# Kernel optimization log

Hardware: AMD Instinct MI355X
Metric: run time of the kernel (lower is better)

## Reference

```python
import jax, jax.numpy as jnp
import numpy as np

B, L, D = 2, 2048, 512
H, HD = 8, 64          # num_heads, head_dim (hidden_dim = 512)
WINDOW = 256
SCALE = float(np.sqrt(HD))
LN_EPS = 1e-5


def setup_inputs() -> dict:
    key = jax.random.key(0)
    ks = jax.random.split(key, 10)
    sequence = jax.random.normal(ks[0], (B, L, D), dtype=jnp.float32)
    # lengths in [L - WINDOW//2, L] so no query row is fully masked (avoids NaN, matches original's valid regime)
    sequence_lengths = jax.random.randint(ks[1], (B,), L - WINDOW // 2, L + 1, dtype=jnp.int32)
    timestamps = jnp.sort(jax.random.uniform(ks[2], (B, L), dtype=jnp.float32) * float(L), axis=-1)
    w_std = 0.02
    Wq = jax.random.normal(ks[3], (H * HD, D), dtype=jnp.float32) * w_std
    Wk = jax.random.normal(ks[4], (H * HD, D), dtype=jnp.float32) * w_std
    Wv = jax.random.normal(ks[5], (H * HD, D), dtype=jnp.float32) * w_std
    Wo = jax.random.normal(ks[6], (D, H * HD), dtype=jnp.float32) * w_std
    bo = jnp.zeros((D,), dtype=jnp.float32)
    ln_gamma = jnp.ones((D,), dtype=jnp.float32)
    ln_beta = jnp.zeros((D,), dtype=jnp.float32)
    temporal_weight = jnp.array([0.1], dtype=jnp.float32)
    return {
        "sequence": sequence, "sequence_lengths": sequence_lengths, "timestamps": timestamps,
        "ln_gamma": ln_gamma, "ln_beta": ln_beta,
        "Wq": Wq, "Wk": Wk, "Wv": Wv, "Wo": Wo, "bo": bo,
        "temporal_weight": temporal_weight,
    }


def reference(sequence, sequence_lengths, timestamps, ln_gamma, ln_beta,
              Wq, Wk, Wv, Wo, bo, temporal_weight):
    residual = sequence
    # LayerNorm over input_dim
    mu = jnp.mean(sequence, axis=-1, keepdims=True)
    var = jnp.mean(jnp.square(sequence - mu), axis=-1, keepdims=True)
    x = (sequence - mu) * jax.lax.rsqrt(var + LN_EPS) * ln_gamma + ln_beta

    # QKV projections (spectral-normalized Linear, no bias) -> [B, L, H, HD]
    Q = (x @ Wq.T).reshape(B, L, H, HD)
    K = (x @ Wk.T).reshape(B, L, H, HD)
    V = (x @ Wv.T).reshape(B, L, H, HD)

    scores = jnp.einsum("bqhd,bkhd->bhqk", Q, K) / SCALE  # [B, H, L, L]

    # temporal decay bias
    ts_diff = jnp.abs(timestamps[:, :, None] - timestamps[:, None, :])  # [B, L, L]
    temporal_weights = jnp.exp(-jnp.abs(temporal_weight[0]) * ts_diff)
    scores = scores + jnp.log(temporal_weights + 1e-8)[:, None, :, :]

    neg_inf = jnp.float32(-jnp.inf)
    # sliding window mask (L > window_size): |i - j| <= window_size // 2
    idx = jnp.arange(L)
    wmask = jnp.abs(idx[None, :] - idx[:, None]) <= WINDOW // 2  # [L, L]
    scores = jnp.where(wmask[None, None, :, :], scores, neg_inf)

    # padding mask on key positions
    pmask = idx[None, :] < sequence_lengths[:, None]  # [B, L]
    scores = jnp.where(pmask[:, None, None, :], scores, neg_inf)

    attn = jax.nn.softmax(scores, axis=-1)  # [B, H, L, L]
    attended = jnp.einsum("bhqk,bkhd->bqhd", attn, V).reshape(B, L, H * HD)

    output = attended @ Wo.T + bo + residual  # [B, L, D]

    # exponential position-weighted aggregation over valid positions
    pos = idx.astype(jnp.float32)
    pw = jnp.exp(-0.1 * (L - 1 - pos))[None, :] * pmask.astype(jnp.float32)  # [B, L]
    pw = pw / (jnp.sum(pw, axis=1, keepdims=True) + 1e-8)
    aggregated = jnp.sum(output * pw[:, :, None], axis=1)  # [B, D]
    return aggregated
```

## Files before the change

### kernel.cpp

```cpp
#include <hip/hip_runtime.h>
#include <math.h>

#define B 2
#define L 2048
#define D 512
#define H 8
#define HD 64
#define W2 128
#define NOUT (3*D)

#define QS 1792
#define NQ (L - QS)
#define ROWS0 (QS - W2)
#define NROWS (L - ROWS0)
#define MROWS (B * NROWS)

#define TQ 4
#define NQT (NQ / TQ)

typedef __bf16 bf16_t;
typedef __attribute__((ext_vector_type(4))) __bf16 bf16x4;
typedef __attribute__((ext_vector_type(8))) __bf16 bf16x8;
typedef __attribute__((ext_vector_type(4))) float f32x4;

#define PREP_LN_BLOCKS (MROWS / 4)
#define PREP_CVT_BLOCKS 768
#define PREP_AGGS_BLOCKS 16
#define PREP_GRID (PREP_LN_BLOCKS + PREP_CVT_BLOCKS + PREP_AGGS_BLOCKS + 1)

__global__ __launch_bounds__(256) void prep_kernel(const float* __restrict__ seq,
                                                   const float* __restrict__ gamma,
                                                   const float* __restrict__ beta,
                                                   const float* __restrict__ Wq,
                                                   const float* __restrict__ Wk,
                                                   const float* __restrict__ Wv,
                                                   const int* __restrict__ slen,
                                                   bf16_t* __restrict__ xb,
                                                   bf16_t* __restrict__ wb,
                                                   float* __restrict__ aggA,
                                                   float* __restrict__ aggS) {
    int blk = blockIdx.x;
    int tid = threadIdx.x;
    int wid = tid >> 6, lane = tid & 63;

    if (blk < PREP_LN_BLOCKS) {
        int row = blk * 4 + wid;
        int b = row / NROWS;
        int l = ROWS0 + (row - b * NROWS);
        const float* src = seq + ((size_t)b * L + l) * D;
        float4 v0 = ((const float4*)src)[lane];
        float4 v1 = ((const float4*)src)[lane + 64];
        float s  = v0.x + v0.y + v0.z + v0.w + v1.x + v1.y + v1.z + v1.w;
        float sq = v0.x*v0.x + v0.y*v0.y + v0.z*v0.z + v0.w*v0.w
                 + v1.x*v1.x + v1.y*v1.y + v1.z*v1.z + v1.w*v1.w;
        for (int o = 32; o; o >>= 1) { s += __shfl_xor(s, o); sq += __shfl_xor(sq, o); }
        float mu = s * (1.0f / D);
        float var = sq * (1.0f / D) - mu * mu;
        float rstd = rsqrtf(var + 1e-5f);
        float4 g0 = ((const float4*)gamma)[lane];
        float4 g1 = ((const float4*)gamma)[lane + 64];
        float4 b0 = ((const float4*)beta)[lane];
        float4 b1 = ((const float4*)beta)[lane + 64];
        bf16x4 c0, c1;
        c0[0] = (bf16_t)((v0.x - mu) * rstd * g0.x + b0.x);
        c0[1] = (bf16_t)((v0.y - mu) * rstd * g0.y + b0.y);
        c0[2] = (bf16_t)((v0.z - mu) * rstd * g0.z + b0.z);
        c0[3] = (bf16_t)((v0.w - mu) * rstd * g0.w + b0.w);
        c1[0] = (bf16_t)((v1.x - mu) * rstd * g1.x + b1.x);
        c1[1] = (bf16_t)((v1.y - mu) * rstd * g1.y + b1.y);
        c1[2] = (bf16_t)((v1.z - mu) * rstd * g1.z + b1.z);
        c1[3] = (bf16_t)((v1.w - mu) * rstd * g1.w + b1.w);
        bf16x4* dst = (bf16x4*)(xb + (size_t)row * D);
        dst[lane] = c0;
        dst[lane + 64] = c1;
    } else if (blk < PREP_LN_BLOCKS + PREP_CVT_BLOCKS) {
        int idx = (blk - PREP_LN_BLOCKS) * 256 + tid;
        const float* src = (idx < 65536) ? Wq : (idx < 131072 ? Wk : Wv);
        int off = idx & 65535;
        float4 v = ((const float4*)src)[off];
        bf16x4 o;
        o[0] = (bf16_t)v.x; o[1] = (bf16_t)v.y; o[2] = (bf16_t)v.z; o[3] = (bf16_t)v.w;
        ((bf16x4*)wb)[idx] = o;
    } else if (blk < PREP_LN_BLOCKS + PREP_CVT_BLOCKS + PREP_AGGS_BLOCKS) {
        __shared__ float red[4][64];
        int idx = blk - (PREP_LN_BLOCKS + PREP_CVT_BLOCKS);
        int b = idx >> 3;
        int col = (idx & 7) * 64 + lane;
        int nv = slen[b] - QS;
        float s2 = 0.f;
        int i0 = wid * 64, i1 = min(i0 + 64, nv);
        for (int i = i0; i < i1; ++i) {
            float wi = __expf(-0.1f * (float)(NQ - 1 - i));
            s2 += wi * seq[((size_t)(b * L + QS + i)) * D + col];
        }
        red[wid][lane] = s2;
        __syncthreads();
        if (wid == 0) {
            aggS[b * D + col] = red[0][lane] + red[1][lane] + red[2][lane] + red[3][lane];
        }
    } else {
        ((float4*)aggA)[tid & 255] = make_float4(0.f, 0.f, 0.f, 0.f);
    }
}

__global__ __launch_bounds__(256) void qkv_gemm(const bf16_t* __restrict__ xb,
                                                const bf16_t* __restrict__ wb,
                                                float* __restrict__ qkv) {
    int m0 = blockIdx.x * 64, n0 = blockIdx.y * 64;
    int wid = threadIdx.x >> 6, lane = threadIdx.x & 63;
    int mw = m0 + (wid >> 1) * 32;
    int nw = n0 + (wid & 1) * 32;
    int mr = lane & 15, quad = lane >> 4;
    f32x4 acc00 = {}, acc01 = {}, acc10 = {}, acc11 = {};
    const bf16_t* aptr = xb + (size_t)(mw + mr) * D + quad * 8;
    const bf16_t* bptr = wb + (size_t)(nw + mr) * D + quad * 8;
#pragma unroll 4
    for (int k = 0; k < D; k += 32) {
        bf16x8 a0 = *(const bf16x8*)(aptr + k);
        bf16x8 a1 = *(const bf16x8*)(aptr + 16 * D + k);
        bf16x8 b0 = *(const bf16x8*)(bptr + k);
        bf16x8 b1 = *(const bf16x8*)(bptr + 16 * D + k);
        acc00 = __builtin_amdgcn_mfma_f32_16x16x32_bf16(a0, b0, acc00, 0, 0, 0);
        acc01 = __builtin_amdgcn_mfma_f32_16x16x32_bf16(a0, b1, acc01, 0, 0, 0);
        acc10 = __builtin_amdgcn_mfma_f32_16x16x32_bf16(a1, b0, acc10, 0, 0, 0);
        acc11 = __builtin_amdgcn_mfma_f32_16x16x32_bf16(a1, b1, acc11, 0, 0, 0);
    }
    float* base = qkv + (size_t)(mw + quad * 4) * NOUT + nw + mr;
#pragma unroll
    for (int r = 0; r < 4; ++r) {
        base[(size_t)r * NOUT +  0] = acc00[r];
        base[(size_t)r * NOUT + 16] = acc01[r];
        base[(size_t)(16 + r) * NOUT +  0] = acc10[r];
        base[(size_t)(16 + r) * NOUT + 16] = acc11[r];
    }
}

__global__ __launch_bounds__(256) void attn_kernel(const float* __restrict__ qkv,
                                                   const float* __restrict__ ts,
                                                   const int* __restrict__ slen,
                                                   const float* __restrict__ tw,
                                                   float* __restrict__ aggA) {
    int bid = blockIdx.x;
    int b = bid / (NQT * H);
    int rem = bid - b * (NQT * H);
    int qt = rem / H;
    int h = rem - qt * H;
    int wid = threadIdx.x >> 6;
    int lane = threadIdx.x & 63;
    int q0 = QS + qt * TQ;
    int sl = slen[b];
    if (q0 >= sl) return;
    int kmin = q0 - W2;
    int kmax = min(q0 + TQ - 1 + W2, sl - 1);
    int nk = kmax - kmin + 1;
    int chunk = (nk + 3) >> 2;
    int start = wid * chunk;
    int end = min(start + chunk, nk);
    int cnt = max(end - start, 0);

    __shared__ __attribute__((aligned(16))) float qv[TQ][HD];
    __shared__ __attribute__((aligned(16))) float p[4][66][TQ];
    __shared__ __attribute__((aligned(16))) float pacc[4][TQ][HD];
    __shared__ float mlm[4][TQ];
    __shared__ float mll[4][TQ];
    __shared__ float tqs[TQ];

    {
        int row = b * NROWS + (q0 + wid - ROWS0);
        qv[wid][lane] = qkv[(size_t)row * NOUT + h * HD + lane];
        if (lane == 0) tqs[wid] = ts[b * L + q0 + wid];
    }
    __syncthreads();

    float atw = fabsf(tw[0]);

    float m[TQ] = {-INFINITY, -INFINITY, -INFINITY, -INFINITY};
    float sreg[2][TQ];
#pragma unroll
    for (int it = 0; it < 2; ++it) {
        int kk = start + it * 64 + lane;
        bool act = (kk < end);
        float s[TQ] = {0.f, 0.f, 0.f, 0.f};
        if (act) {
            int k = kmin + kk;
            const float* Krow = qkv + (size_t)(b * NROWS + k - ROWS0) * NOUT + D + h * HD;
#pragma unroll
            for (int d4 = 0; d4 < 16; ++d4) {
                float4 kv = ((const float4*)Krow)[d4];
#pragma unroll
                for (int t = 0; t < TQ; ++t) {
                    float4 qq = *(const float4*)&qv[t][d4 * 4];
                    s[t] += qq.x * kv.x + qq.y * kv.y + qq.z * kv.z + qq.w * kv.w;
                }
            }
            float tk = ts[b * L + k];
#pragma unroll
            for (int t = 0; t < TQ; ++t) {
                float dt = fabsf(tqs[t] - tk);
                float bias = logf(expf(-atw * dt) + 1e-8f);
                int qa = q0 + t;
                bool valid = (k >= qa - W2) && (k <= qa + W2);
                s[t] = valid ? (s[t] * 0.125f + bias) : -INFINITY;
            }
        } else {
#pragma unroll
            for (int t = 0; t < TQ; ++t) s[t] = -INFINITY;
        }
#pragma unroll
        for (int t = 0; t < TQ; ++t) { sreg[it][t] = s[t]; m[t] = fmaxf(m[t], s[t]); }
    }
#pragma unroll
    for (int t = 0; t < TQ; ++t)
        for (int o = 32; o; o >>= 1) m[t] = fmaxf(m[t], __shfl_xor(m[t], o));

    float l[TQ] = {0.f, 0.f, 0.f, 0.f};
#pragma unroll
    for (int it = 0; it < 2; ++it) {
        int kk = start + it * 64 + lane;
        bool act = (kk < end);
        float pv[TQ];
#pragma unroll
        for (int t = 0; t < TQ; ++t) {
            float pp = (m[t] > -INFINITY) ? expf(sreg[it][t] - m[t]) : 0.0f;
            pv[t] = pp;
            l[t] += act ? pp : 0.0f;
        }
        if (act) {
            *(float4*)&p[wid][kk - start][0] = make_float4(pv[0], pv[1], pv[2], pv[3]);
        }
    }
#pragma unroll
    for (int t = 0; t < TQ; ++t)
        for (int o = 32; o; o >>= 1) l[t] += __shfl_xor(l[t], o);
    if (lane == 0) {
#pragma unroll
        for (int t = 0; t < TQ; ++t) { mlm[wid][t] = m[t]; mll[wid][t] = l[t]; }
    }

    float acc[TQ] = {0.f, 0.f, 0.f, 0.f};
    const float* Vbase = qkv + (size_t)(b * NROWS + kmin + start - ROWS0) * NOUT + 2 * D + h * HD + lane;
#pragma unroll 4
    for (int kl = 0; kl < cnt; ++kl) {
        float v = Vbase[(size_t)kl * NOUT];
        float4 pp = *(const float4*)&p[wid][kl][0];
        acc[0] += pp.x * v; acc[1] += pp.y * v; acc[2] += pp.z * v; acc[3] += pp.w * v;
    }
#pragma unroll
    for (int t = 0; t < TQ; ++t) pacc[wid][t][lane] = acc[t];
    __syncthreads();

    {
        int t = wid;
        int q = q0 + t;
        if (q < sl) {
            float m0 = mlm[0][t], m1 = mlm[1][t], m2 = mlm[2][t], m3 = mlm[3][t];
            float M = fmaxf(fmaxf(m0, m1), fmaxf(m2, m3));
            float e0 = expf(m0 - M), e1 = expf(m1 - M), e2 = expf(m2 - M), e3 = expf(m3 - M);
            float Lsum = e0 * mll[0][t] + e1 * mll[1][t] + e2 * mll[2][t] + e3 * mll[3][t];
            float o = e0 * pacc[0][t][lane] + e1 * pacc[1][t][lane]
                    + e2 * pacc[2][t][lane] + e3 * pacc[3][t][lane];
            float wq = __expf(-0.1f * (float)(L - 1 - q));
            atomicAdd(&aggA[b * D + h * HD + lane], (o / Lsum) * wq);
        }
    }
}

__global__ __launch_bounds__(64) void out_kernel(const float* __restrict__ aggA,
                                                 const float* __restrict__ aggS,
                                                 const float* __restrict__ Wo,
                                                 const float* __restrict__ bo,
                                                 const int* __restrict__ slen,
                                                 float* __restrict__ out) {
    int bid = blockIdx.x;
    int b = bid >> 9;
    int d = bid & 511;
    int lane = threadIdx.x;
    int nv = slen[b] - QS;
    float den = 0.f;
#pragma unroll
    for (int j = 0; j < 4; ++j) {
        int i = lane * 4 + j;
        den += (i < nv) ? __expf(-0.1f * (float)(NQ - 1 - i)) : 0.0f;
    }
    for (int o = 32; o; o >>= 1) den += __shfl_xor(den, o);

    const float* wrow = Wo + (size_t)d * D;
    const float* arow = aggA + b * D;
    float acc = 0.0f;
#pragma unroll
    for (int i = 0; i < 8; ++i) {
        int j = lane + 64 * i;
        acc += arow[j] * wrow[j];
    }
    for (int o = 32; o; o >>= 1) acc += __shfl_xor(acc, o);
    if (lane == 0) {
        float inv = 1.0f / (den + 1e-8f);
        out[b * D + d] = (acc + aggS[b * D + d] + bo[d] * den) * inv;
    }
}

extern "C" void kernel_launch(void* const* d_in, const int* in_sizes, int n_in,
                              void* d_out, int out_size, void* d_ws, size_t ws_size,
                              hipStream_t stream) {
    const float* seq   = (const float*)d_in[0];
    const int*   slen  = (const int*)d_in[1];
    const float* ts    = (const float*)d_in[2];
    const float* gamma = (const float*)d_in[3];
    const float* beta  = (const float*)d_in[4];
    const float* Wq    = (const float*)d_in[5];
    const float* Wk    = (const float*)d_in[6];
    const float* Wv    = (const float*)d_in[7];
    const float* Wo    = (const float*)d_in[8];
    const float* bo    = (const float*)d_in[9];
    const float* tw    = (const float*)d_in[10];
    float* out = (float*)d_out;

    float* ws   = (float*)d_ws;
    float* qkv  = ws;
    float* aggA = qkv + (size_t)MROWS * NOUT;
    float* aggS = aggA + B * D;
    bf16_t* xb  = (bf16_t*)(aggS + B * D);
    bf16_t* wb  = xb + (size_t)MROWS * D;

    prep_kernel<<<PREP_GRID, 256, 0, stream>>>(seq, gamma, beta, Wq, Wk, Wv, slen,
                                               xb, wb, aggA, aggS);
    dim3 ggrid(MROWS / 64, NOUT / 64);
    qkv_gemm<<<ggrid, 256, 0, stream>>>(xb, wb, qkv);
    attn_kernel<<<B * NQT * H, 256, 0, stream>>>(qkv, ts, slen, tw, aggA);
    out_kernel<<<B * D, 64, 0, stream>>>(aggA, aggS, Wo, bo, slen, out);
}
```

Measured before the change: 130.2 us.

## Store Q/K/V as per-head bf16 tensors and parallelize tail aggregation with atomics

The QKV GEMM now writes bf16 outputs into separate head-major Q, K and V buffers instead of one interleaved fp32 buffer. This halves the intermediate traffic and makes each head's K/V rows contiguous for the attention kernel. The GEMM tile shrinks to 32 rows, doubling the block count, and the residual aggregation uses more blocks that combine partial sums with atomicAdd after a memset. Storing Q/K/V in bf16 reduces their precision, and the atomics make the summation order nondeterministic.

```diff
diff --git a/kernel.cpp b/kernel.cpp
--- a/kernel.cpp
+++ b/kernel.cpp
@@ -25,8 +25,8 @@
 
 #define PREP_LN_BLOCKS (MROWS / 4)
 #define PREP_CVT_BLOCKS 768
-#define PREP_AGGS_BLOCKS 16
-#define PREP_GRID (PREP_LN_BLOCKS + PREP_CVT_BLOCKS + PREP_AGGS_BLOCKS + 1)
+#define PREP_AGGS_BLOCKS 64
+#define PREP_GRID (PREP_LN_BLOCKS + PREP_CVT_BLOCKS + PREP_AGGS_BLOCKS)
 
 __global__ __launch_bounds__(256) void prep_kernel(const float* __restrict__ seq,
                                                    const float* __restrict__ gamma,
@@ -37,7 +37,6 @@
                                                    const int* __restrict__ slen,
                                                    bf16_t* __restrict__ xb,
                                                    bf16_t* __restrict__ wb,
-                                                   float* __restrict__ aggA,
                                                    float* __restrict__ aggS) {
     int blk = blockIdx.x;
     int tid = threadIdx.x;
@@ -81,61 +80,63 @@
         bf16x4 o;
         o[0] = (bf16_t)v.x; o[1] = (bf16_t)v.y; o[2] = (bf16_t)v.z; o[3] = (bf16_t)v.w;
         ((bf16x4*)wb)[idx] = o;
-    } else if (blk < PREP_LN_BLOCKS + PREP_CVT_BLOCKS + PREP_AGGS_BLOCKS) {
-        __shared__ float red[4][64];
+    } else {
         int idx = blk - (PREP_LN_BLOCKS + PREP_CVT_BLOCKS);
-        int b = idx >> 3;
-        int col = (idx & 7) * 64 + lane;
+        int b = idx >> 5;
+        int rc = (idx >> 3) & 3;
+        int ct = idx & 7;
+        int col = ct * 64 + lane;
         int nv = slen[b] - QS;
+        int i0 = rc * 64 + wid * 16;
+        int i1 = min(i0 + 16, nv);
         float s2 = 0.f;
-        int i0 = wid * 64, i1 = min(i0 + 64, nv);
+#pragma unroll 4
         for (int i = i0; i < i1; ++i) {
-            float wi = __expf(-0.1f * (float)(NQ - 1 - i));
-            s2 += wi * seq[((size_t)(b * L + QS + i)) * D + col];
-        }
-        red[wid][lane] = s2;
-        __syncthreads();
-        if (wid == 0) {
-            aggS[b * D + col] = red[0][lane] + red[1][lane] + red[2][lane] + red[3][lane];
-        }
-    } else {
-        ((float4*)aggA)[tid & 255] = make_float4(0.f, 0.f, 0.f, 0.f);
+            s2 += __expf(-0.1f * (float)(NQ - 1 - i)) * seq[((size_t)(b * L + QS + i)) * D + col];
+        }
+        if (i1 > i0) atomicAdd(&aggS[b * D + col], s2);
     }
 }
 
 __global__ __launch_bounds__(256) void qkv_gemm(const bf16_t* __restrict__ xb,
                                                 const bf16_t* __restrict__ wb,
-                                                float* __restrict__ qkv) {
-    int m0 = blockIdx.x * 64, n0 = blockIdx.y * 64;
+                                                bf16_t* __restrict__ Qb,
+                                                bf16_t* __restrict__ Kb,
+                                                bf16_t* __restrict__ Vb) {
+    int m0 = blockIdx.x * 32, n0 = blockIdx.y * 64;
     int wid = threadIdx.x >> 6, lane = threadIdx.x & 63;
-    int mw = m0 + (wid >> 1) * 32;
+    int mw = m0 + (wid >> 1) * 16;
     int nw = n0 + (wid & 1) * 32;
     int mr = lane & 15, quad = lane >> 4;
-    f32x4 acc00 = {}, acc01 = {}, acc10 = {}, acc11 = {};
+    f32x4 acc0 = {}, acc1 = {};
     const bf16_t* aptr = xb + (size_t)(mw + mr) * D + quad * 8;
     const bf16_t* bptr = wb + (size_t)(nw + mr) * D + quad * 8;
-#pragma unroll 4
+#pragma unroll 8
     for (int k = 0; k < D; k += 32) {
-        bf16x8 a0 = *(const bf16x8*)(aptr + k);
-        bf16x8 a1 = *(const bf16x8*)(aptr + 16 * D + k);
+        bf16x8 a  = *(const bf16x8*)(aptr + k);
         bf16x8 b0 = *(const bf16x8*)(bptr + k);
         bf16x8 b1 = *(const bf16x8*)(bptr + 16 * D + k);
-        acc00 = __builtin_amdgcn_mfma_f32_16x16x32_bf16(a0, b0, acc00, 0, 0, 0);
-        acc01 = __builtin_amdgcn_mfma_f32_16x16x32_bf16(a0, b1, acc01, 0, 0, 0);
-        acc10 = __builtin_amdgcn_mfma_f32_16x16x32_bf16(a1, b0, acc10, 0, 0, 0);
-        acc11 = __builtin_amdgcn_mfma_f32_16x16x32_bf16(a1, b1, acc11, 0, 0, 0);
-    }
-    float* base = qkv + (size_t)(mw + quad * 4) * NOUT + nw + mr;
-#pragma unroll
-    for (int r = 0; r < 4; ++r) {
-        base[(size_t)r * NOUT +  0] = acc00[r];
-        base[(size_t)r * NOUT + 16] = acc01[r];
-        base[(size_t)(16 + r) * NOUT +  0] = acc10[r];
-        base[(size_t)(16 + r) * NOUT + 16] = acc11[r];
-    }
-}
-
-__global__ __launch_bounds__(256) void attn_kernel(const float* __restrict__ qkv,
+        acc0 = __builtin_amdgcn_mfma_f32_16x16x32_bf16(a, b0, acc0, 0, 0, 0);
+        acc1 = __builtin_amdgcn_mfma_f32_16x16x32_bf16(a, b1, acc1, 0, 0, 0);
+    }
+    int sec = n0 >> 9;
+    int h = (n0 >> 6) & 7;
+    int d0 = nw & 63;
+    bf16_t* dstbase = (sec == 0) ? Qb : (sec == 1 ? Kb : Vb);
+    int m = mw + quad * 4;
+    int b = m / NROWS;
+    int r = m - b * NROWS;
+    bf16_t* dst = dstbase + ((size_t)(b * H + h) * NROWS + r) * HD + d0 + mr;
+#pragma unroll
+    for (int rr = 0; rr < 4; ++rr) {
+        dst[(size_t)rr * HD]      = (bf16_t)acc0[rr];
+        dst[(size_t)rr * HD + 16] = (bf16_t)acc1[rr];
+    }
+}
+
+__global__ __launch_bounds__(256) void attn_kernel(const bf16_t* __restrict__ Qb,
+                                                   const bf16_t* __restrict__ Kb,
+                                                   const bf16_t* __restrict__ Vb,
                                                    const float* __restrict__ ts,
                                                    const int* __restrict__ slen,
                                                    const float* __restrict__ tw,
@@ -165,9 +166,11 @@
     __shared__ float mll[4][TQ];
     __shared__ float tqs[TQ];
 
+    const size_t headbase = (size_t)(b * H + h) * NROWS;
+
     {
-        int row = b * NROWS + (q0 + wid - ROWS0);
-        qv[wid][lane] = qkv[(size_t)row * NOUT + h * HD + lane];
+        int qr = q0 + wid - ROWS0;
+        qv[wid][lane] = (float)Qb[(headbase + qr) * HD + lane];
         if (lane == 0) tqs[wid] = ts[b * L + q0 + wid];
     }
     __syncthreads();
@@ -183,14 +186,17 @@
         float s[TQ] = {0.f, 0.f, 0.f, 0.f};
         if (act) {
             int k = kmin + kk;
-            const float* Krow = qkv + (size_t)(b * NROWS + k - ROWS0) * NOUT + D + h * HD;
-#pragma unroll
-            for (int d4 = 0; d4 < 16; ++d4) {
-                float4 kv = ((const float4*)Krow)[d4];
+            const bf16_t* Krow = Kb + (headbase + (k - ROWS0)) * HD;
+#pragma unroll
+            for (int d8 = 0; d8 < 8; ++d8) {
+                bf16x8 kv = *(const bf16x8*)(Krow + d8 * 8);
+                float kf0 = (float)kv[0], kf1 = (float)kv[1], kf2 = (float)kv[2], kf3 = (float)kv[3];
+                float kf4 = (float)kv[4], kf5 = (float)kv[5], kf6 = (float)kv[6], kf7 = (float)kv[7];
 #pragma unroll
                 for (int t = 0; t < TQ; ++t) {
-                    float4 qq = *(const float4*)&qv[t][d4 * 4];
-                    s[t] += qq.x * kv.x + qq.y * kv.y + qq.z * kv.z + qq.w * kv.w;
+                    const float* qq = &qv[t][d8 * 8];
+                    s[t] += qq[0]*kf0 + qq[1]*kf1 + qq[2]*kf2 + qq[3]*kf3
+                          + qq[4]*kf4 + qq[5]*kf5 + qq[6]*kf6 + qq[7]*kf7;
                 }
             }
             float tk = ts[b * L + k];
@@ -238,10 +244,10 @@
     }
 
     float acc[TQ] = {0.f, 0.f, 0.f, 0.f};
-    const float* Vbase = qkv + (size_t)(b * NROWS + kmin + start - ROWS0) * NOUT + 2 * D + h * HD + lane;
+    const bf16_t* Vbase = Vb + (headbase + (kmin + start - ROWS0)) * HD + lane;
 #pragma unroll 4
     for (int kl = 0; kl < cnt; ++kl) {
-        float v = Vbase[(size_t)kl * NOUT];
+        float v = (float)Vbase[(size_t)kl * HD];
         float4 pp = *(const float4*)&p[wid][kl][0];
         acc[0] += pp.x * v; acc[1] += pp.y * v; acc[2] += pp.z * v; acc[3] += pp.w * v;
     }
@@ -315,17 +321,20 @@
     const float* tw    = (const float*)d_in[10];
     float* out = (float*)d_out;
 
-    float* ws   = (float*)d_ws;
-    float* qkv  = ws;
-    float* aggA = qkv + (size_t)MROWS * NOUT;
-    float* aggS = aggA + B * D;
-    bf16_t* xb  = (bf16_t*)(aggS + B * D);
-    bf16_t* wb  = xb + (size_t)MROWS * D;
-
+    float* ws    = (float*)d_ws;
+    float* aggA  = ws;
+    float* aggS  = aggA + B * D;
+    bf16_t* xb   = (bf16_t*)(aggS + B * D);
+    bf16_t* wb   = xb + (size_t)MROWS * D;
+    bf16_t* Qb   = wb + (size_t)NOUT * D;
+    bf16_t* Kb   = Qb + (size_t)B * H * NROWS * HD;
+    bf16_t* Vb   = Kb + (size_t)B * H * NROWS * HD;
+
+    hipMemsetAsync(aggA, 0, 2 * B * D * sizeof(float), stream);
     prep_kernel<<<PREP_GRID, 256, 0, stream>>>(seq, gamma, beta, Wq, Wk, Wv, slen,
-                                               xb, wb, aggA, aggS);
-    dim3 ggrid(MROWS / 64, NOUT / 64);
-    qkv_gemm<<<ggrid, 256, 0, stream>>>(xb, wb, qkv);
-    attn_kernel<<<B * NQT * H, 256, 0, stream>>>(qkv, ts, slen, tw, aggA);
+                                               xb, wb, aggS);
+    dim3 ggrid(MROWS / 32, NOUT / 64);
+    qkv_gemm<<<ggrid, 256, 0, stream>>>(xb, wb, Qb, Kb, Vb);
+    attn_kernel<<<B * NQT * H, 256, 0, stream>>>(Qb, Kb, Vb, ts, slen, tw, aggA);
     out_kernel<<<B * D, 64, 0, stream>>>(aggA, aggS, Wo, bo, slen, out);
 }
```

After: 119.9 us. 1.09x faster.
